# Kernel tuning notes

Hardware: AMD Instinct MI355X
Metric: run time of the kernel (lower is better)

The kernel has to match this reference:

```python
import jax, jax.numpy as jnp
import numpy as np

N = 100_000      # nodes
E = 1_600_000    # edges (avg degree 16)
P = 100_000      # pos/neg sampled edges
L = 3            # GIN layers
D_IN = 128
D_H = 128
D_MLP = 512
D_PRED = D_H // 2
D_FIN = 1


def setup_inputs() -> dict:
    key = jax.random.key(0)
    ks = jax.random.split(key, 12)
    s_in = 1.0 / np.sqrt(D_IN)
    s_mlp = 1.0 / np.sqrt(D_MLP)
    s_h = 1.0 / np.sqrt(D_H)
    s_p = 1.0 / np.sqrt(D_PRED)
    return {
        "x":   jax.random.normal(ks[0], (N, D_IN), jnp.float32),
        "W1":  jax.random.normal(ks[1], (L, D_IN, D_MLP), jnp.float32) * s_in,
        "b1":  jnp.zeros((L, D_MLP), jnp.float32),
        "W2":  jax.random.normal(ks[2], (L, D_MLP, D_H), jnp.float32) * s_mlp,
        "b2":  jnp.zeros((L, D_H), jnp.float32),
        "Wp1": jax.random.normal(ks[3], (D_H, D_PRED), jnp.float32) * s_h,
        "bp1": jnp.zeros((D_PRED,), jnp.float32),
        "Wp2": jax.random.normal(ks[4], (D_PRED, D_FIN), jnp.float32) * s_p,
        "bp2": jnp.zeros((D_FIN,), jnp.float32),
        "edge_src": jax.random.randint(ks[5], (E,), 0, N),
        "edge_dst": jax.random.randint(ks[6], (E,), 0, N),
        "pos_src": jax.random.randint(ks[7], (P,), 0, N),
        "pos_dst": jax.random.randint(ks[8], (P,), 0, N),
        "neg_src": jax.random.randint(ks[9], (P,), 0, N),
        "neg_dst": jax.random.randint(ks[10], (P,), 0, N),
    }


def reference(x, W1, b1, W2, b2, Wp1, bp1, Wp2, bp2,
              edge_src, edge_dst, pos_src, pos_dst, neg_src, neg_dst):
    h = x
    for l in range(L):
        # GINConv 'sum': aggregate neighbor features src->dst, eps=0
        agg = jax.ops.segment_sum(h[edge_src], edge_dst, num_segments=N)
        z = jax.nn.relu((h + agg) @ W1[l] + b1[l])   # [N, D_MLP]
        h = z @ W2[l] + b2[l]                        # [N, D_H]
        h = jax.nn.relu(h)                           # outer ReLU in forward()

    def predict(src, dst):
        z = jax.nn.relu((h[src] * h[dst]) @ Wp1 + bp1)
        return z @ Wp2 + bp2                         # [P, D_FIN]

    h_pos = predict(pos_src, pos_dst)
    h_neg = predict(neg_src, neg_dst)
    return (h_pos, h_neg, h)
```

## Files before the change

### kernel.cpp

```cpp
#include <hip/hip_runtime.h>

typedef unsigned short ushort_t;

constexpr int NN = 100000;
constexpr int EE = 1600000;
constexpr int PP = 100000;
constexpr int DH = 128;
constexpr int DM = 512;

using frag_b16 = __attribute__((ext_vector_type(8))) short;
using frag_f32 = __attribute__((ext_vector_type(4))) float;

union FragU {
  ushort_t s[8];
  uint4 u;
  frag_b16 f;
};

__device__ inline void split_bf16(float x, ushort_t& hi, ushort_t& lo) {
  unsigned int bx = __float_as_uint(x);
  hi = (ushort_t)(bx >> 16);
  float hf = __uint_as_float(bx & 0xFFFF0000u);
  float r = x - hf;
  unsigned int br = __float_as_uint(r);
  unsigned int rb = br + 0x7FFFu + ((br >> 16) & 1u);
  lo = (ushort_t)(rb >> 16);
}

__device__ inline ushort_t rne_bf16(float x) {
  unsigned int u = __float_as_uint(x);
  unsigned int r = u + 0x7FFFu + ((u >> 16) & 1u);
  return (ushort_t)(r >> 16);
}

__device__ inline void bf2x(unsigned int u, float& a, float& b) {
  a = __uint_as_float(u << 16);
  b = __uint_as_float(u & 0xFFFF0000u);
}

__device__ inline void g2l16(const ushort_t* __restrict__ g, ushort_t* l) {
  __builtin_amdgcn_global_load_lds(
      (const __attribute__((address_space(1))) void*)g,
      (__attribute__((address_space(3))) void*)l, 16, 0, 0);
}


__global__ void hist_kernel(const int* __restrict__ dst, int* __restrict__ deg) {
  int i = blockIdx.x * 256 + threadIdx.x;
  if (i < EE) atomicAdd(&deg[dst[i]], 1);
}

__global__ void scan1_kernel(const int* __restrict__ deg, int* __restrict__ inc,
                             int* __restrict__ bsum) {
  __shared__ int buf[2][512];
  int base = blockIdx.x * 512;
  for (int i = threadIdx.x; i < 512; i += 256) {
    int g = base + i;
    buf[0][i] = (g < NN) ? deg[g] : 0;
  }
  __syncthreads();
  int cur = 0;
  for (int off = 1; off < 512; off <<= 1) {
    int nxt = cur ^ 1;
    for (int i = threadIdx.x; i < 512; i += 256) {
      int v = buf[cur][i];
      if (i >= off) v += buf[cur][i - off];
      buf[nxt][i] = v;
    }
    __syncthreads();
    cur = nxt;
  }
  for (int i = threadIdx.x; i < 512; i += 256) {
    int g = base + i;
    if (g < NN) inc[g] = buf[cur][i];
  }
  if (threadIdx.x == 0) bsum[blockIdx.x] = buf[cur][511];
}

__global__ void scan2_kernel(int* __restrict__ bsum, int nb) {
  __shared__ int buf[2][256];
  int i = threadIdx.x;
  buf[0][i] = (i < nb) ? bsum[i] : 0;
  __syncthreads();
  int cur = 0;
  for (int off = 1; off < 256; off <<= 1) {
    int nxt = cur ^ 1;
    int v = buf[cur][i];
    if (i >= off) v += buf[cur][i - off];
    buf[nxt][i] = v;
    __syncthreads();
    cur = nxt;
  }
  if (i < nb) bsum[i] = (i == 0) ? 0 : buf[cur][i - 1];
}

__global__ void scan3_kernel(const int* __restrict__ inc, const int* __restrict__ deg,
                             const int* __restrict__ bsum,
                             int* __restrict__ row_off, int* __restrict__ cursor) {
  int i = blockIdx.x * 256 + threadIdx.x;
  if (i < NN) {
    int excl = inc[i] - deg[i] + bsum[i >> 9];
    row_off[i] = excl;
    cursor[i] = excl;
    if (i == NN - 1) row_off[NN] = excl + deg[i];
  }
}

constexpr int SC_NW = 8;
constexpr int SC_WND = (NN + SC_NW - 1) / SC_NW;
constexpr int SC_EPB = 8192;
constexpr int SC_CHUNKS = (EE + SC_EPB - 1) / SC_EPB;

__global__ __launch_bounds__(256) void scatter_kernel(const int* __restrict__ esrc,
                                                      const int* __restrict__ edst,
                                                      int* __restrict__ cursor,
                                                      int* __restrict__ csr) {
  const int w = blockIdx.x & (SC_NW - 1);
  const int chunk = blockIdx.x / SC_NW;
  const int lo = w * SC_WND;
  const int hi = lo + SC_WND;
  const int base = chunk * SC_EPB;
  #pragma unroll 4
  for (int it = 0; it < SC_EPB / 256; ++it) {
    int i = base + it * 256 + threadIdx.x;
    if (i < EE) {
      int d = edst[i];
      if (d >= lo && d < hi) {
        int p = atomicAdd(&cursor[d], 1);
        csr[p] = esrc[i];
      }
    }
  }
}

__global__ void pack_w1_kernel(const float* __restrict__ W1, ushort_t* __restrict__ wp) {
  int t = blockIdx.x * 256 + threadIdx.x;
  if (t >= 3 * 128 * 64) return;
  int lane = t & 63;
  int tile = t >> 6;
  int tk = tile & 3;
  int tn = (tile >> 2) & 31;
  int layer = tile >> 7;
  int n = tn * 16 + (lane & 15);
  int k0 = tk * 32 + (lane >> 4) * 8;
  const float* src = W1 + (size_t)layer * DH * DM;
  size_t dst = (size_t)t * 8;
  #pragma unroll
  for (int j = 0; j < 8; ++j) wp[dst + j] = rne_bf16(src[(size_t)(k0 + j) * DM + n]);
}

__global__ void pack_w2_kernel(const float* __restrict__ W2, ushort_t* __restrict__ wp) {
  int t = blockIdx.x * 256 + threadIdx.x;
  if (t >= 3 * 128 * 64) return;
  int lane = t & 63;
  int tile = t >> 6;
  int tn = tile & 7;
  int ktg = (tile >> 3) & 15;
  int layer = tile >> 7;
  int n = tn * 16 + (lane & 15);
  int k0 = ktg * 32 + (lane >> 4) * 8;
  const float* src = W2 + (size_t)layer * DM * DH;
  size_t dst = (size_t)t * 8;
  #pragma unroll
  for (int j = 0; j < 8; ++j) wp[dst + j] = rne_bf16(src[(size_t)(k0 + j) * DH + n]);
}

__global__ void pack_wp1_kernel(const float* __restrict__ Wp1, ushort_t* __restrict__ wp) {
  int t = blockIdx.x * 256 + threadIdx.x;
  if (t >= 16 * 64) return;
  int lane = t & 63;
  int tile = t >> 6;
  int tn = tile & 3;
  int tk = tile >> 2;
  int n = tn * 16 + (lane & 15);
  int k0 = tk * 32 + (lane >> 4) * 8;
  size_t dst = (size_t)t * 8;
  #pragma unroll
  for (int j = 0; j < 8; ++j) wp[dst + j] = rne_bf16(Wp1[(size_t)(k0 + j) * 64 + n]);
}

__global__ void cvt_bf16_kernel(const float* __restrict__ x, ushort_t* __restrict__ xb) {
  int i = blockIdx.x * 256 + threadIdx.x;
  if (i < NN * DH / 4) {
    float4 v = ((const float4*)x)[i];
    ushort4 o;
    o.x = rne_bf16(v.x); o.y = rne_bf16(v.y); o.z = rne_bf16(v.z); o.w = rne_bf16(v.w);
    ((ushort4*)xb)[i] = o;
  }
}

__global__ __launch_bounds__(256) void agg_kernel(const ushort_t* __restrict__ hbf,
                                                  const int* __restrict__ row_off,
                                                  const int* __restrict__ csr,
                                                  ushort_t* __restrict__ s_hi,
                                                  ushort_t* __restrict__ s_lo) {
  int t = blockIdx.x * 256 + threadIdx.x;
  int grp = t >> 4;
  int lane = t & 15;
  if (grp >= NN) return;
  const uint4* hp = (const uint4*)hbf;
  float acc[8];
  {
    uint4 v = hp[(size_t)grp * 16 + lane];
    bf2x(v.x, acc[0], acc[1]);
    bf2x(v.y, acc[2], acc[3]);
    bf2x(v.z, acc[4], acc[5]);
    bf2x(v.w, acc[6], acc[7]);
  }
  int e = row_off[grp];
  int e1 = row_off[grp + 1];
  for (; e + 1 < e1; e += 2) {
    uint4 a = hp[(size_t)csr[e] * 16 + lane];
    uint4 b = hp[(size_t)csr[e + 1] * 16 + lane];
    float f0, f1;
    bf2x(a.x, f0, f1); acc[0] += f0; acc[1] += f1;
    bf2x(a.y, f0, f1); acc[2] += f0; acc[3] += f1;
    bf2x(a.z, f0, f1); acc[4] += f0; acc[5] += f1;
    bf2x(a.w, f0, f1); acc[6] += f0; acc[7] += f1;
    bf2x(b.x, f0, f1); acc[0] += f0; acc[1] += f1;
    bf2x(b.y, f0, f1); acc[2] += f0; acc[3] += f1;
    bf2x(b.z, f0, f1); acc[4] += f0; acc[5] += f1;
    bf2x(b.w, f0, f1); acc[6] += f0; acc[7] += f1;
  }
  if (e < e1) {
    uint4 a = hp[(size_t)csr[e] * 16 + lane];
    float f0, f1;
    bf2x(a.x, f0, f1); acc[0] += f0; acc[1] += f1;
    bf2x(a.y, f0, f1); acc[2] += f0; acc[3] += f1;
    bf2x(a.z, f0, f1); acc[4] += f0; acc[5] += f1;
    bf2x(a.w, f0, f1); acc[6] += f0; acc[7] += f1;
  }
  unsigned int hw[4], lw[4];
  #pragma unroll
  for (int i = 0; i < 4; ++i) {
    ushort_t h0, l0, h1, l1;
    split_bf16(acc[2 * i], h0, l0);
    split_bf16(acc[2 * i + 1], h1, l1);
    hw[i] = (unsigned int)h0 | ((unsigned int)h1 << 16);
    lw[i] = (unsigned int)l0 | ((unsigned int)l1 << 16);
  }
  size_t o = (size_t)grp * DH + lane * 8;
  *(uint4*)(s_hi + o) = make_uint4(hw[0], hw[1], hw[2], hw[3]);
  *(uint4*)(s_lo + o) = make_uint4(lw[0], lw[1], lw[2], lw[3]);
}

__global__ __launch_bounds__(256, 4) void mlp_kernel(
    const ushort_t* __restrict__ s_hi, const ushort_t* __restrict__ s_lo,
    const ushort_t* __restrict__ w1p, const float* __restrict__ b1s,
    const ushort_t* __restrict__ w2p, const float* __restrict__ b2s,
    float* __restrict__ hout_f32, ushort_t* __restrict__ hout_bf16) {
  __shared__ ushort_t wA[8 * 512];
  __shared__ ushort_t wB[8 * 512];
  __shared__ float zt[32 * 66];
  const int tid = threadIdx.x;
  const int wave = tid >> 6;
  const int lane = tid & 63;
  const int quad = lane >> 4;
  const int l15 = lane & 15;
  const int m_base = wave * 16;
  const int row0 = blockIdx.x * 64;

  frag_b16 a_hi[4], a_lo[4];
  {
    int gr = row0 + m_base + l15;
    if (gr >= NN) gr = NN - 1;
    #pragma unroll
    for (int tk = 0; tk < 4; ++tk) {
      size_t o = (size_t)gr * DH + tk * 32 + quad * 8;
      FragU uh, ul;
      uh.u = *(const uint4*)(s_hi + o);
      ul.u = *(const uint4*)(s_lo + o);
      a_hi[tk] = uh.f;
      a_lo[tk] = ul.f;
    }
  }

  frag_f32 hacc[8];
  #pragma unroll
  for (int tn = 0; tn < 8; ++tn) hacc[tn] = {0.f, 0.f, 0.f, 0.f};

  for (int ch = 0; ch < 16; ++ch) {
    #pragma unroll
    for (int i = 0; i < 2; ++i)
      g2l16(w1p + ((size_t)(ch * 512 + i * 256 + tid)) * 8, wA + (i * 256 + tid) * 8);
    #pragma unroll
    for (int i = 0; i < 2; ++i)
      g2l16(w2p + ((size_t)(ch * 512 + i * 256 + tid)) * 8, wB + (i * 256 + tid) * 8);
    __syncthreads();

    frag_f32 za[2];
    #pragma unroll
    for (int tn = 0; tn < 2; ++tn) za[tn] = {0.f, 0.f, 0.f, 0.f};

    #pragma unroll
    for (int tk = 0; tk < 4; ++tk) {
      #pragma unroll
      for (int tn = 0; tn < 2; ++tn) {
        FragU wv;
        wv.u = *(const uint4*)(wA + (tn * 4 + tk) * 512 + lane * 8);
        za[tn] = __builtin_amdgcn_mfma_f32_16x16x32_bf16(a_hi[tk], wv.f, za[tn], 0, 0, 0);
        za[tn] = __builtin_amdgcn_mfma_f32_16x16x32_bf16(a_lo[tk], wv.f, za[tn], 0, 0, 0);
      }
    }

    #pragma unroll
    for (int tn = 0; tn < 2; ++tn) {
      float b1v = b1s[ch * 32 + tn * 16 + l15];
      float z0 = fmaxf(za[tn][0] + b1v, 0.f);
      float z1 = fmaxf(za[tn][1] + b1v, 0.f);
      float z2 = fmaxf(za[tn][2] + b1v, 0.f);
      float z3 = fmaxf(za[tn][3] + b1v, 0.f);
      float* zp = &zt[(tn * 16 + l15) * 66 + m_base + quad * 4];
      *(float2*)zp = make_float2(z0, z1);
      *(float2*)(zp + 2) = make_float2(z2, z3);
    }

    FragU zh, zl;
    #pragma unroll
    for (int j = 0; j < 8; ++j) {
      float v = zt[(quad * 8 + j) * 66 + m_base + l15];
      split_bf16(v, zh.s[j], zl.s[j]);
    }
    #pragma unroll
    for (int tn = 0; tn < 8; ++tn) {
      FragU wv;
      wv.u = *(const uint4*)(wB + tn * 512 + lane * 8);
      hacc[tn] = __builtin_amdgcn_mfma_f32_16x16x32_bf16(zh.f, wv.f, hacc[tn], 0, 0, 0);
      hacc[tn] = __builtin_amdgcn_mfma_f32_16x16x32_bf16(zl.f, wv.f, hacc[tn], 0, 0, 0);
    }
    __syncthreads();
  }

  #pragma unroll
  for (int tn = 0; tn < 8; ++tn) {
    int col = tn * 16 + l15;
    float b2v = b2s[col];
    #pragma unroll
    for (int r = 0; r < 4; ++r) {
      int gr = row0 + m_base + quad * 4 + r;
      if (gr < NN) {
        float v = fmaxf(hacc[tn][r] + b2v, 0.f);
        if (hout_f32) hout_f32[(size_t)gr * DH + col] = v;
        if (hout_bf16) hout_bf16[(size_t)gr * DH + col] = rne_bf16(v);
      }
    }
  }
}

__global__ __launch_bounds__(256, 2) void predict_kernel(
    const float* __restrict__ h, const int* __restrict__ psrc, const int* __restrict__ pdst,
    const int* __restrict__ nsrc, const int* __restrict__ ndst,
    const ushort_t* __restrict__ wp1p, const float* __restrict__ bp1,
    const float* __restrict__ Wp2, const float* __restrict__ bp2,
    float* __restrict__ out) {
  __shared__ unsigned int gp[128 * 128];
  const int tid = threadIdx.x;
  const int wave = tid >> 6;
  const int lane = tid & 63;
  const int quad = lane >> 4;
  const int l15 = lane & 15;
  const int m_base = wave * 32;
  const int s0 = blockIdx.x * 128;

  FragU wb1[4][4];
  #pragma unroll
  for (int tk = 0; tk < 4; ++tk)
    #pragma unroll
    for (int tn = 0; tn < 4; ++tn)
      wb1[tk][tn].u = *(const uint4*)(wp1p + ((size_t)((tk * 4 + tn) * 64 + lane)) * 8);

  #pragma unroll 8
  for (int i = 0; i < 16; ++i) {
    int idx = tid + i * 256;
    int m = idx >> 5;
    int c4 = (idx & 31) << 2;
    int smp = s0 + m;
    uint4 pk = make_uint4(0u, 0u, 0u, 0u);
    if (smp < 2 * PP) {
      int si = (smp < PP) ? psrc[smp] : nsrc[smp - PP];
      int di = (smp < PP) ? pdst[smp] : ndst[smp - PP];
      float4 a = *(const float4*)(h + (size_t)si * DH + c4);
      float4 b = *(const float4*)(h + (size_t)di * DH + c4);
      ushort_t hh, ll;
      split_bf16(a.x * b.x, hh, ll); pk.x = (unsigned)hh | ((unsigned)ll << 16);
      split_bf16(a.y * b.y, hh, ll); pk.y = (unsigned)hh | ((unsigned)ll << 16);
      split_bf16(a.z * b.z, hh, ll); pk.z = (unsigned)hh | ((unsigned)ll << 16);
      split_bf16(a.w * b.w, hh, ll); pk.w = (unsigned)hh | ((unsigned)ll << 16);
    }
    int slot = (m << 7) + c4;
    slot ^= (m & 7) << 2;
    *(uint4*)(gp + slot) = pk;
  }
  __syncthreads();

  frag_f32 za[2][4];
  #pragma unroll
  for (int ms = 0; ms < 2; ++ms)
    #pragma unroll
    for (int tn = 0; tn < 4; ++tn) za[ms][tn] = {0.f, 0.f, 0.f, 0.f};

  #pragma unroll
  for (int ms = 0; ms < 2; ++ms) {
    int m = m_base + ms * 16 + l15;
    int swz = (m & 7) << 2;
    #pragma unroll
    for (int tk = 0; tk < 4; ++tk) {
      int idx0 = (m << 7) + tk * 32 + quad * 8;
      uint4 u0 = *(const uint4*)(gp + (idx0 ^ swz));
      uint4 u1 = *(const uint4*)(gp + ((idx0 + 4) ^ swz));
      unsigned int uu[8];
      *(uint4*)uu = u0;
      *(uint4*)(uu + 4) = u1;
      FragU ah, al;
      #pragma unroll
      for (int j = 0; j < 8; ++j) {
        ah.s[j] = (ushort_t)(uu[j] & 0xFFFFu);
        al.s[j] = (ushort_t)(uu[j] >> 16);
      }
      #pragma unroll
      for (int tn = 0; tn < 4; ++tn) {
        za[ms][tn] = __builtin_amdgcn_mfma_f32_16x16x32_bf16(ah.f, wb1[tk][tn].f,
                                                             za[ms][tn], 0, 0, 0);
        za[ms][tn] = __builtin_amdgcn_mfma_f32_16x16x32_bf16(al.f, wb1[tk][tn].f,
                                                             za[ms][tn], 0, 0, 0);
      }
    }
  }

  float b1v[4], w2v[4];
  #pragma unroll
  for (int tn = 0; tn < 4; ++tn) {
    b1v[tn] = bp1[tn * 16 + l15];
    w2v[tn] = Wp2[tn * 16 + l15];
  }
  float bias = bp2[0];
  #pragma unroll
  for (int ms = 0; ms < 2; ++ms) {
    #pragma unroll
    for (int r = 0; r < 4; ++r) {
      float p = 0.f;
      #pragma unroll
      for (int tn = 0; tn < 4; ++tn)
        p += fmaxf(za[ms][tn][r] + b1v[tn], 0.f) * w2v[tn];
      p += __shfl_xor(p, 1, 64);
      p += __shfl_xor(p, 2, 64);
      p += __shfl_xor(p, 4, 64);
      p += __shfl_xor(p, 8, 64);
      if (l15 == 0) {
        int smp = s0 + m_base + ms * 16 + quad * 4 + r;
        if (smp < 2 * PP) out[smp] = p + bias;
      }
    }
  }
}

extern "C" void kernel_launch(void* const* d_in, const int* in_sizes, int n_in,
                              void* d_out, int out_size, void* d_ws, size_t ws_size,
                              hipStream_t stream) {
  const float* x   = (const float*)d_in[0];
  const float* W1  = (const float*)d_in[1];
  const float* b1  = (const float*)d_in[2];
  const float* W2  = (const float*)d_in[3];
  const float* b2  = (const float*)d_in[4];
  const float* Wp1 = (const float*)d_in[5];
  const float* bp1 = (const float*)d_in[6];
  const float* Wp2 = (const float*)d_in[7];
  const float* bp2 = (const float*)d_in[8];
  const int* esrc = (const int*)d_in[9];
  const int* edst = (const int*)d_in[10];
  const int* psrc = (const int*)d_in[11];
  const int* pdst = (const int*)d_in[12];
  const int* nsrc = (const int*)d_in[13];
  const int* ndst = (const int*)d_in[14];

  float* out = (float*)d_out;
  float* out_pred = out;
  float* hbuf = out + 2 * (size_t)PP;
  ushort_t* hbf = (ushort_t*)hbuf;

  char* w = (char*)d_ws;
  ushort_t* s_hi = (ushort_t*)w;
  ushort_t* s_lo = s_hi + (size_t)NN * DH;
  ushort_t* w1p  = s_lo + (size_t)NN * DH;
  ushort_t* w2p  = w1p + 3 * 128 * 64 * 8;
  ushort_t* wp1p = w2p + 3 * 128 * 64 * 8;
  int* row_off = (int*)(wp1p + 16 * 64 * 8);
  int* csr     = row_off + (NN + 1);
  int* deg    = (int*)w;
  int* inc    = deg + NN;
  int* bsum   = inc + NN;
  int* cursor = bsum + 256;

  hipMemsetAsync(deg, 0, NN * sizeof(int), stream);
  hist_kernel<<<(EE + 255) / 256, 256, 0, stream>>>(edst, deg);
  scan1_kernel<<<(NN + 511) / 512, 256, 0, stream>>>(deg, inc, bsum);
  scan2_kernel<<<1, 256, 0, stream>>>(bsum, (NN + 511) / 512);
  scan3_kernel<<<(NN + 255) / 256, 256, 0, stream>>>(inc, deg, bsum, row_off, cursor);
  scatter_kernel<<<SC_CHUNKS * SC_NW, 256, 0, stream>>>(esrc, edst, cursor, csr);

  pack_w1_kernel<<<96, 256, 0, stream>>>(W1, w1p);
  pack_w2_kernel<<<96, 256, 0, stream>>>(W2, w2p);
  pack_wp1_kernel<<<4, 256, 0, stream>>>(Wp1, wp1p);

  cvt_bf16_kernel<<<(NN * DH / 4 + 255) / 256, 256, 0, stream>>>(x, hbf);

  for (int l = 0; l < 3; ++l) {
    agg_kernel<<<(NN * 16 + 255) / 256, 256, 0, stream>>>(hbf, row_off, csr, s_hi, s_lo);
    mlp_kernel<<<(NN + 63) / 64, 256, 0, stream>>>(
        s_hi, s_lo,
        w1p + (size_t)l * 128 * 64 * 8, b1 + (size_t)l * DM,
        w2p + (size_t)l * 128 * 64 * 8, b2 + (size_t)l * DH,
        (l == 2) ? hbuf : nullptr, (l == 2) ? nullptr : hbf);
  }

  predict_kernel<<<(2 * PP + 127) / 128, 256, 0, stream>>>(
      hbuf, psrc, pdst, nsrc, ndst, wp1p, bp1, Wp2, bp2, out_pred);
}
```

Before: 735.2 us.

## Fuse neighbor aggregation into the GIN MLP kernel via shared-memory staging

The separate aggregation kernel is removed. Each MLP block now gathers and sums neighbor features for its own 64 rows, splits the sums into hi/lo bf16, and stages them through XOR-swizzled shared memory that reuses the weight buffers before loading MFMA fragments. This avoids writing and re-reading the hi/lo aggregate arrays in global memory and saves one launch per layer. Because layers can no longer update features in place, hidden features ping-pong between two bf16 buffers. The cost is that the gather now runs inside a kernel with occupancy limited by launch_bounds(256,4), so there is less latency hiding for the irregular loads, and extra barriers are added.

```diff
diff --git a/kernel.cpp b/kernel.cpp
--- a/kernel.cpp
+++ b/kernel.cpp
@@ -189,69 +189,17 @@
   }
 }
 
-__global__ __launch_bounds__(256) void agg_kernel(const ushort_t* __restrict__ hbf,
-                                                  const int* __restrict__ row_off,
-                                                  const int* __restrict__ csr,
-                                                  ushort_t* __restrict__ s_hi,
-                                                  ushort_t* __restrict__ s_lo) {
-  int t = blockIdx.x * 256 + threadIdx.x;
-  int grp = t >> 4;
-  int lane = t & 15;
-  if (grp >= NN) return;
-  const uint4* hp = (const uint4*)hbf;
-  float acc[8];
-  {
-    uint4 v = hp[(size_t)grp * 16 + lane];
-    bf2x(v.x, acc[0], acc[1]);
-    bf2x(v.y, acc[2], acc[3]);
-    bf2x(v.z, acc[4], acc[5]);
-    bf2x(v.w, acc[6], acc[7]);
-  }
-  int e = row_off[grp];
-  int e1 = row_off[grp + 1];
-  for (; e + 1 < e1; e += 2) {
-    uint4 a = hp[(size_t)csr[e] * 16 + lane];
-    uint4 b = hp[(size_t)csr[e + 1] * 16 + lane];
-    float f0, f1;
-    bf2x(a.x, f0, f1); acc[0] += f0; acc[1] += f1;
-    bf2x(a.y, f0, f1); acc[2] += f0; acc[3] += f1;
-    bf2x(a.z, f0, f1); acc[4] += f0; acc[5] += f1;
-    bf2x(a.w, f0, f1); acc[6] += f0; acc[7] += f1;
-    bf2x(b.x, f0, f1); acc[0] += f0; acc[1] += f1;
-    bf2x(b.y, f0, f1); acc[2] += f0; acc[3] += f1;
-    bf2x(b.z, f0, f1); acc[4] += f0; acc[5] += f1;
-    bf2x(b.w, f0, f1); acc[6] += f0; acc[7] += f1;
-  }
-  if (e < e1) {
-    uint4 a = hp[(size_t)csr[e] * 16 + lane];
-    float f0, f1;
-    bf2x(a.x, f0, f1); acc[0] += f0; acc[1] += f1;
-    bf2x(a.y, f0, f1); acc[2] += f0; acc[3] += f1;
-    bf2x(a.z, f0, f1); acc[4] += f0; acc[5] += f1;
-    bf2x(a.w, f0, f1); acc[6] += f0; acc[7] += f1;
-  }
-  unsigned int hw[4], lw[4];
-  #pragma unroll
-  for (int i = 0; i < 4; ++i) {
-    ushort_t h0, l0, h1, l1;
-    split_bf16(acc[2 * i], h0, l0);
-    split_bf16(acc[2 * i + 1], h1, l1);
-    hw[i] = (unsigned int)h0 | ((unsigned int)h1 << 16);
-    lw[i] = (unsigned int)l0 | ((unsigned int)l1 << 16);
-  }
-  size_t o = (size_t)grp * DH + lane * 8;
-  *(uint4*)(s_hi + o) = make_uint4(hw[0], hw[1], hw[2], hw[3]);
-  *(uint4*)(s_lo + o) = make_uint4(lw[0], lw[1], lw[2], lw[3]);
-}
-
-__global__ __launch_bounds__(256, 4) void mlp_kernel(
-    const ushort_t* __restrict__ s_hi, const ushort_t* __restrict__ s_lo,
+__global__ __launch_bounds__(256, 4) void gin_kernel(
+    const ushort_t* __restrict__ hprev,
+    const int* __restrict__ row_off, const int* __restrict__ csr,
     const ushort_t* __restrict__ w1p, const float* __restrict__ b1s,
     const ushort_t* __restrict__ w2p, const float* __restrict__ b2s,
     float* __restrict__ hout_f32, ushort_t* __restrict__ hout_bf16) {
-  __shared__ ushort_t wA[8 * 512];
-  __shared__ ushort_t wB[8 * 512];
+  __shared__ uint4 smemq[1024];
   __shared__ float zt[32 * 66];
+  char* smem = (char*)smemq;
+  ushort_t* wA = (ushort_t*)smemq;
+  ushort_t* wB = (ushort_t*)(smemq + 512);
   const int tid = threadIdx.x;
   const int wave = tid >> 6;
   const int lane = tid & 63;
@@ -261,18 +209,73 @@
   const int row0 = blockIdx.x * 64;
 
   frag_b16 a_hi[4], a_lo[4];
-  {
-    int gr = row0 + m_base + l15;
-    if (gr >= NN) gr = NN - 1;
-    #pragma unroll
-    for (int tk = 0; tk < 4; ++tk) {
-      size_t o = (size_t)gr * DH + tk * 32 + quad * 8;
-      FragU uh, ul;
-      uh.u = *(const uint4*)(s_hi + o);
-      ul.u = *(const uint4*)(s_lo + o);
-      a_hi[tk] = uh.f;
-      a_lo[tk] = ul.f;
-    }
+  const uint4* hp = (const uint4*)hprev;
+  #pragma unroll 1
+  for (int b = 0; b < 2; ++b) {
+    #pragma unroll 1
+    for (int half = 0; half < 2; ++half) {
+      int rl = (tid >> 4) + half * 16;
+      int lane16 = tid & 15;
+      int gr = row0 + b * 32 + rl;
+      int grc = (gr < NN) ? gr : NN - 1;
+      float acc[8];
+      {
+        uint4 v = hp[(size_t)grc * 16 + lane16];
+        bf2x(v.x, acc[0], acc[1]);
+        bf2x(v.y, acc[2], acc[3]);
+        bf2x(v.z, acc[4], acc[5]);
+        bf2x(v.w, acc[6], acc[7]);
+      }
+      int e = row_off[grc];
+      int e1 = row_off[grc + 1];
+      for (; e + 1 < e1; e += 2) {
+        uint4 a = hp[(size_t)csr[e] * 16 + lane16];
+        uint4 bq = hp[(size_t)csr[e + 1] * 16 + lane16];
+        float f0, f1;
+        bf2x(a.x, f0, f1); acc[0] += f0; acc[1] += f1;
+        bf2x(a.y, f0, f1); acc[2] += f0; acc[3] += f1;
+        bf2x(a.z, f0, f1); acc[4] += f0; acc[5] += f1;
+        bf2x(a.w, f0, f1); acc[6] += f0; acc[7] += f1;
+        bf2x(bq.x, f0, f1); acc[0] += f0; acc[1] += f1;
+        bf2x(bq.y, f0, f1); acc[2] += f0; acc[3] += f1;
+        bf2x(bq.z, f0, f1); acc[4] += f0; acc[5] += f1;
+        bf2x(bq.w, f0, f1); acc[6] += f0; acc[7] += f1;
+      }
+      if (e < e1) {
+        uint4 a = hp[(size_t)csr[e] * 16 + lane16];
+        float f0, f1;
+        bf2x(a.x, f0, f1); acc[0] += f0; acc[1] += f1;
+        bf2x(a.y, f0, f1); acc[2] += f0; acc[3] += f1;
+        bf2x(a.z, f0, f1); acc[4] += f0; acc[5] += f1;
+        bf2x(a.w, f0, f1); acc[6] += f0; acc[7] += f1;
+      }
+      unsigned int hw[4], lw[4];
+      #pragma unroll
+      for (int i = 0; i < 4; ++i) {
+        ushort_t h0, l0, h1, l1;
+        split_bf16(acc[2 * i], h0, l0);
+        split_bf16(acc[2 * i + 1], h1, l1);
+        hw[i] = (unsigned int)h0 | ((unsigned int)h1 << 16);
+        lw[i] = (unsigned int)l0 | ((unsigned int)l1 << 16);
+      }
+      int bo = (rl * 256 + lane16 * 16) ^ ((rl & 7) << 4);
+      *(uint4*)(smem + bo) = make_uint4(hw[0], hw[1], hw[2], hw[3]);
+      *(uint4*)(smem + 8192 + bo) = make_uint4(lw[0], lw[1], lw[2], lw[3]);
+    }
+    __syncthreads();
+    if ((wave >> 1) == b) {
+      int rl = (wave & 1) * 16 + l15;
+      #pragma unroll
+      for (int tk = 0; tk < 4; ++tk) {
+        int bo = (rl * 256 + tk * 64 + quad * 16) ^ ((rl & 7) << 4);
+        FragU uh, ul;
+        uh.u = *(const uint4*)(smem + bo);
+        ul.u = *(const uint4*)(smem + 8192 + bo);
+        a_hi[tk] = uh.f;
+        a_lo[tk] = ul.f;
+      }
+    }
+    __syncthreads();
   }
 
   frag_f32 hacc[8];
@@ -476,12 +479,11 @@
   float* out = (float*)d_out;
   float* out_pred = out;
   float* hbuf = out + 2 * (size_t)PP;
-  ushort_t* hbf = (ushort_t*)hbuf;
 
   char* w = (char*)d_ws;
-  ushort_t* s_hi = (ushort_t*)w;
-  ushort_t* s_lo = s_hi + (size_t)NN * DH;
-  ushort_t* w1p  = s_lo + (size_t)NN * DH;
+  ushort_t* hA   = (ushort_t*)w;
+  ushort_t* hB   = hA + (size_t)NN * DH;
+  ushort_t* w1p  = hB + (size_t)NN * DH;
   ushort_t* w2p  = w1p + 3 * 128 * 64 * 8;
   ushort_t* wp1p = w2p + 3 * 128 * 64 * 8;
   int* row_off = (int*)(wp1p + 16 * 64 * 8);
@@ -502,16 +504,18 @@
   pack_w2_kernel<<<96, 256, 0, stream>>>(W2, w2p);
   pack_wp1_kernel<<<4, 256, 0, stream>>>(Wp1, wp1p);
 
-  cvt_bf16_kernel<<<(NN * DH / 4 + 255) / 256, 256, 0, stream>>>(x, hbf);
-
-  for (int l = 0; l < 3; ++l) {
-    agg_kernel<<<(NN * 16 + 255) / 256, 256, 0, stream>>>(hbf, row_off, csr, s_hi, s_lo);
-    mlp_kernel<<<(NN + 63) / 64, 256, 0, stream>>>(
-        s_hi, s_lo,
-        w1p + (size_t)l * 128 * 64 * 8, b1 + (size_t)l * DM,
-        w2p + (size_t)l * 128 * 64 * 8, b2 + (size_t)l * DH,
-        (l == 2) ? hbuf : nullptr, (l == 2) ? nullptr : hbf);
-  }
+  cvt_bf16_kernel<<<(NN * DH / 4 + 255) / 256, 256, 0, stream>>>(x, hA);
+
+  const int GB = (NN + 63) / 64;
+  gin_kernel<<<GB, 256, 0, stream>>>(hA, row_off, csr,
+      w1p + 0 * (size_t)128 * 64 * 8, b1 + 0 * (size_t)DM,
+      w2p + 0 * (size_t)128 * 64 * 8, b2 + 0 * (size_t)DH, nullptr, hB);
+  gin_kernel<<<GB, 256, 0, stream>>>(hB, row_off, csr,
+      w1p + 1 * (size_t)128 * 64 * 8, b1 + 1 * (size_t)DM,
+      w2p + 1 * (size_t)128 * 64 * 8, b2 + 1 * (size_t)DH, nullptr, hA);
+  gin_kernel<<<GB, 256, 0, stream>>>(hA, row_off, csr,
+      w1p + 2 * (size_t)128 * 64 * 8, b1 + 2 * (size_t)DM,
+      w2p + 2 * (size_t)128 * 64 * 8, b2 + 2 * (size_t)DH, hbuf, nullptr);
 
   predict_kernel<<<(2 * PP + 127) / 128, 256, 0, stream>>>(
       hbuf, psrc, pdst, nsrc, ndst, wp1p, bp1, Wp2, bp2, out_pred);
```

Result: slower. 763.3 us (+3.8%).
